# Kernel tuning notes

Measured on AMD Instinct MI355X. Metric: run time of the kernel, lower is better.

Reference implementation:

```python
import jax, jax.numpy as jnp
import numpy as np

B, D, O = 512, 256, 256
H = [512, 1024, 1024]

def _linear_params(key, fan_in, fan_out):
    kw, kb = jax.random.split(key)
    bound = 1.0 / np.sqrt(fan_in)
    W = jax.random.uniform(kw, (fan_out, fan_in), jnp.float32, -bound, bound)
    b = jax.random.uniform(kb, (fan_out,), jnp.float32, -bound, bound)
    return W, b

def setup_inputs() -> dict:
    key = jax.random.key(0)
    ks = jax.random.split(key, 7)
    input_values = jax.random.normal(ks[0], (B, D), jnp.float32)
    nan_flag = jax.random.uniform(ks[1], (B, D), jnp.float32)
    W_in, b_in = _linear_params(ks[2], D, H[0])          # input_layer: nan_flag_dim -> H[0]
    W_h1, b_h1 = _linear_params(ks[3], H[0], H[1])        # hidden layer 1
    W_h2, b_h2 = _linear_params(ks[4], H[1], H[2])        # hidden layer 2
    W_d, b_d = _linear_params(ks[5], H[2], D * O)         # output_branch_dense
    W_b, b_b = _linear_params(ks[6], H[2], O)             # output_branch_bias
    return {"input_values": input_values, "nan_flag": nan_flag, "training": False,
            "W_in": W_in, "b_in": b_in, "W_h1": W_h1, "b_h1": b_h1,
            "W_h2": W_h2, "b_h2": b_h2, "W_d": W_d, "b_d": b_d,
            "W_b": W_b, "b_b": b_b}

def reference(input_values, nan_flag, training, W_in, b_in, W_h1, b_h1, W_h2, b_h2, W_d, b_d, W_b, b_b):
    # training=False: dropout is identity, sample_missing branch skipped (default False)
    x = jax.nn.relu(nan_flag @ W_in.T + b_in)
    x = jax.nn.relu(x @ W_h1.T + b_h1)
    x = jax.nn.relu(x @ W_h2.T + b_h2)
    # per-sample compensation weights [B, D, O] and bias [B, O]
    comp_w = (x @ W_d.T + b_d).reshape(B, D, O)
    comp_b = x @ W_b.T + b_b
    # baddbmm: [B,1,D] @ [B,D,O] + [B,1,O] -> squeeze -> [B,O]
    out = comp_b + jnp.einsum('bd,bdo->bo', input_values, comp_w)
    return out
```

## Files before the change

### kernel.cpp

```cpp
#include <hip/hip_runtime.h>
#include <hip/hip_bf16.h>

#define B_  512
#define D_  256
#define O_  256
#define H2_ 1024

typedef __attribute__((ext_vector_type(4))) float  f32x4;
typedef __attribute__((ext_vector_type(8))) short  short8;
typedef __attribute__((ext_vector_type(4))) short  short4v;

union S8u { short4v v; unsigned u[2]; };

__device__ __forceinline__ unsigned f32_bf16(float x) {
  unsigned u = __builtin_bit_cast(unsigned, x);
  return (u + 0x7fffu + ((u >> 16) & 1u)) >> 16;
}
__device__ __forceinline__ unsigned cvt_pk_bf16(float a, float b) {
  return f32_bf16(a) | (f32_bf16(b) << 16);
}

template <int RELU>
__global__ __launch_bounds__(256)
void gemm_bt64(const float* __restrict__ A, const float* __restrict__ Bm,
               const float* __restrict__ bias, float* __restrict__ C,
               int M, int N, int K) {
  __shared__ __align__(16) short As[64][72];
  __shared__ __align__(16) short Bs[64][72];
  const int t    = threadIdx.x;
  const int m0   = blockIdx.y * 64;
  const int n0   = blockIdx.x * 64;
  const int f4c  = t & 15;
  const int rg   = t >> 4;
  const int lane = t & 63;
  const int w    = t >> 6;
  const int wm   = (w & 1) * 32;
  const int wn   = (w >> 1) * 32;
  const int lr   = lane & 15;
  const int lq   = lane >> 4;

  f32x4 acc[2][2];
  #pragma unroll
  for (int i = 0; i < 2; ++i)
    #pragma unroll
    for (int j = 0; j < 2; ++j) acc[i][j] = f32x4{0.f, 0.f, 0.f, 0.f};

  for (int k0 = 0; k0 < K; k0 += 64) {
    #pragma unroll
    for (int j = 0; j < 4; ++j) {
      int r = rg + 16 * j;
      f32x4 av = *(const f32x4*)(A  + (size_t)(m0 + r) * K + k0 + f4c * 4);
      f32x4 bv = *(const f32x4*)(Bm + (size_t)(n0 + r) * K + k0 + f4c * 4);
      S8u sa; sa.u[0] = cvt_pk_bf16(av.x, av.y); sa.u[1] = cvt_pk_bf16(av.z, av.w);
      S8u sb; sb.u[0] = cvt_pk_bf16(bv.x, bv.y); sb.u[1] = cvt_pk_bf16(bv.z, bv.w);
      *(short4v*)&As[r][f4c * 4] = sa.v;
      *(short4v*)&Bs[r][f4c * 4] = sb.v;
    }
    __syncthreads();
    #pragma unroll
    for (int ks = 0; ks < 2; ++ks) {
      short8 a0 = *(const short8*)&As[wm + lr     ][ks * 32 + lq * 8];
      short8 a1 = *(const short8*)&As[wm + 16 + lr][ks * 32 + lq * 8];
      short8 b0 = *(const short8*)&Bs[wn + lr     ][ks * 32 + lq * 8];
      short8 b1 = *(const short8*)&Bs[wn + 16 + lr][ks * 32 + lq * 8];
      acc[0][0] = __builtin_amdgcn_mfma_f32_16x16x32_bf16(a0, b0, acc[0][0], 0, 0, 0);
      acc[0][1] = __builtin_amdgcn_mfma_f32_16x16x32_bf16(a0, b1, acc[0][1], 0, 0, 0);
      acc[1][0] = __builtin_amdgcn_mfma_f32_16x16x32_bf16(a1, b0, acc[1][0], 0, 0, 0);
      acc[1][1] = __builtin_amdgcn_mfma_f32_16x16x32_bf16(a1, b1, acc[1][1], 0, 0, 0);
    }
    __syncthreads();
  }
  #pragma unroll
  for (int mi = 0; mi < 2; ++mi)
    #pragma unroll
    for (int ni = 0; ni < 2; ++ni)
      #pragma unroll
      for (int r = 0; r < 4; ++r) {
        int row = m0 + wm + mi * 16 + lq * 4 + r;
        int col = n0 + wn + ni * 16 + lr;
        float v = acc[mi][ni][r] + bias[col];
        if (RELU) v = fmaxf(v, 0.f);
        C[(size_t)row * N + col] = v;
      }
}

__global__ __launch_bounds__(256)
void bias_d_kernel(const float* __restrict__ inp, const float* __restrict__ b_d,
                   float* __restrict__ out) {
  const int b = blockIdx.x;
  const int o = threadIdx.x;
  const float* ir = inp + (size_t)b * D_;
  float s = 0.f;
  for (int d = 0; d < D_; ++d)
    s += ir[d] * b_d[(size_t)d * O_ + o];
  out[(size_t)b * O_ + o] += s;
}

__global__ __launch_bounds__(256, 2)
void stage_b(const float* __restrict__ x2, const float* __restrict__ inp,
             const float* __restrict__ Wd, float* __restrict__ out) {
  __shared__ __align__(16) short As[128][72];
  __shared__ __align__(16) short Bs[128][72];
  const int t    = threadIdx.x;
  const int mt   = blockIdx.x >> 1;
  const int nt   = blockIdx.x & 1;
  const int d0   = blockIdx.y * 4;
  const int bm   = mt * 128;
  const int bn   = nt * 128;
  const int f4c  = t & 15;
  const int rg   = t >> 4;
  const int lane = t & 63;
  const int w    = t >> 6;
  const int wm   = (w & 1) * 64;
  const int wn   = (w >> 1) * 64;
  const int lr   = lane & 15;
  const int lq   = lane >> 4;

  f32x4 acc[4][4];
  #pragma unroll
  for (int mi = 0; mi < 4; ++mi)
    #pragma unroll
    for (int ni = 0; ni < 4; ++ni) acc[mi][ni] = f32x4{0.f, 0.f, 0.f, 0.f};

  for (int dl = 0; dl < 4; ++dl) {
    const int d = d0 + dl;
    float insc[8];
    #pragma unroll
    for (int j = 0; j < 8; ++j)
      insc[j] = inp[(size_t)(bm + rg + 16 * j) * D_ + d];
    const float* wbase = Wd + ((size_t)d * O_ + bn) * H2_;

    for (int h0 = 0; h0 < H2_; h0 += 64) {
      #pragma unroll
      for (int j = 0; j < 8; ++j) {
        int r = rg + 16 * j;
        f32x4 xv = *(const f32x4*)(x2 + (size_t)(bm + r) * H2_ + h0 + f4c * 4);
        float s = insc[j];
        S8u sa;
        sa.u[0] = cvt_pk_bf16(xv.x * s, xv.y * s);
        sa.u[1] = cvt_pk_bf16(xv.z * s, xv.w * s);
        *(short4v*)&As[r][f4c * 4] = sa.v;
        f32x4 wv = *(const f32x4*)(wbase + (size_t)r * H2_ + h0 + f4c * 4);
        S8u sb; sb.u[0] = cvt_pk_bf16(wv.x, wv.y); sb.u[1] = cvt_pk_bf16(wv.z, wv.w);
        *(short4v*)&Bs[r][f4c * 4] = sb.v;
      }
      __syncthreads();
      #pragma unroll
      for (int ks = 0; ks < 2; ++ks) {
        short8 af[4], bfr[4];
        #pragma unroll
        for (int mi = 0; mi < 4; ++mi)
          af[mi] = *(const short8*)&As[wm + mi * 16 + lr][ks * 32 + lq * 8];
        #pragma unroll
        for (int ni = 0; ni < 4; ++ni)
          bfr[ni] = *(const short8*)&Bs[wn + ni * 16 + lr][ks * 32 + lq * 8];
        #pragma unroll
        for (int mi = 0; mi < 4; ++mi)
          #pragma unroll
          for (int ni = 0; ni < 4; ++ni)
            acc[mi][ni] = __builtin_amdgcn_mfma_f32_16x16x32_bf16(af[mi], bfr[ni],
                                                                  acc[mi][ni], 0, 0, 0);
      }
      __syncthreads();
    }
  }

  #pragma unroll
  for (int mi = 0; mi < 4; ++mi)
    #pragma unroll
    for (int ni = 0; ni < 4; ++ni)
      #pragma unroll
      for (int r = 0; r < 4; ++r) {
        int row = bm + wm + mi * 16 + lq * 4 + r;
        int col = bn + wn + ni * 16 + lr;
        atomicAdd(out + (size_t)row * O_ + col, acc[mi][ni][r]);
      }
}

extern "C" void kernel_launch(void* const* d_in, const int* in_sizes, int n_in,
                              void* d_out, int out_size, void* d_ws, size_t ws_size,
                              hipStream_t stream) {
  const float* input = (const float*)d_in[0];
  const float* nanf  = (const float*)d_in[1];
  const float* W_in  = (const float*)d_in[3];
  const float* b_in  = (const float*)d_in[4];
  const float* W_h1  = (const float*)d_in[5];
  const float* b_h1  = (const float*)d_in[6];
  const float* W_h2  = (const float*)d_in[7];
  const float* b_h2  = (const float*)d_in[8];
  const float* W_d   = (const float*)d_in[9];
  const float* b_d   = (const float*)d_in[10];
  const float* W_b   = (const float*)d_in[11];
  const float* b_b   = (const float*)d_in[12];
  float* out = (float*)d_out;

  float* x0 = (float*)d_ws;
  float* x1 = x0 + 512 * 512;
  float* x2 = x1 + 512 * 1024;

  gemm_bt64<1><<<dim3(512 / 64, 512 / 64), 256, 0, stream>>>(nanf, W_in, b_in, x0, 512, 512, 256);
  gemm_bt64<1><<<dim3(1024 / 64, 512 / 64), 256, 0, stream>>>(x0, W_h1, b_h1, x1, 512, 1024, 512);
  gemm_bt64<1><<<dim3(1024 / 64, 512 / 64), 256, 0, stream>>>(x1, W_h2, b_h2, x2, 512, 1024, 1024);
  gemm_bt64<0><<<dim3(256 / 64, 512 / 64), 256, 0, stream>>>(x2, W_b, b_b, out, 512, 256, 1024);
  bias_d_kernel<<<512, 256, 0, stream>>>(input, b_d, out);
  stage_b<<<dim3(8, 64), 256, 0, stream>>>(x2, input, W_d, out);
}
```

Baseline: 630.3 us.

## Pre-convert W_d and x2 to bf16 and stream via global_load_lds in stage_b

Adds a conversion kernel that turns W_d (256 MB fp32) and x2 into bf16 copies in the workspace each call. The main stage then loads tiles directly into LDS with global_load_lds instead of converting fp32 in registers. The input scaling moves from the A operand to a per-d epilogue that accumulates scaled partial results. The conversion pass reads all of W_d and writes a 128 MB copy, which adds traffic unless it is cheaper than the fp32 reads it replaces. The fast path only runs if the workspace is large enough, otherwise the old kernel is used.

After: 647.9 us. +2.8%, slower.

```diff
diff --git a/kernel.cpp b/kernel.cpp
--- a/kernel.cpp
+++ b/kernel.cpp
@@ -1,5 +1,4 @@
 #include <hip/hip_runtime.h>
-#include <hip/hip_bf16.h>
 
 #define B_  512
 #define D_  256
@@ -9,8 +8,10 @@
 typedef __attribute__((ext_vector_type(4))) float  f32x4;
 typedef __attribute__((ext_vector_type(8))) short  short8;
 typedef __attribute__((ext_vector_type(4))) short  short4v;
-
-union S8u { short4v v; unsigned u[2]; };
+typedef unsigned short ushort_t;
+
+union S8u  { short4v v; unsigned u[2]; };
+union S16u { short8  v; unsigned u[4]; };
 
 __device__ __forceinline__ unsigned f32_bf16(float x) {
   unsigned u = __builtin_bit_cast(unsigned, x);
@@ -18,6 +19,12 @@
 }
 __device__ __forceinline__ unsigned cvt_pk_bf16(float a, float b) {
   return f32_bf16(a) | (f32_bf16(b) << 16);
+}
+
+__device__ __forceinline__ void gload_lds16(const void* g, void* l) {
+  __builtin_amdgcn_global_load_lds(
+      (const __attribute__((address_space(1))) unsigned*)g,
+      (__attribute__((address_space(3))) unsigned*)l, 16, 0, 0);
 }
 
 template <int RELU>
@@ -96,9 +103,116 @@
   out[(size_t)b * O_ + o] += s;
 }
 
+__global__ __launch_bounds__(256)
+void cvt_f32_bf16(const float* __restrict__ in, ushort_t* __restrict__ out, int n8) {
+  for (size_t i = (size_t)blockIdx.x * 256 + threadIdx.x; i < (size_t)n8;
+       i += (size_t)gridDim.x * 256) {
+    const float* p = in + i * 8;
+    f32x4 v0 = *(const f32x4*)p;
+    f32x4 v1 = *(const f32x4*)(p + 4);
+    S16u s;
+    s.u[0] = cvt_pk_bf16(v0.x, v0.y);
+    s.u[1] = cvt_pk_bf16(v0.z, v0.w);
+    s.u[2] = cvt_pk_bf16(v1.x, v1.y);
+    s.u[3] = cvt_pk_bf16(v1.z, v1.w);
+    *(short8*)(out + i * 8) = s.v;
+  }
+}
+
 __global__ __launch_bounds__(256, 2)
-void stage_b(const float* __restrict__ x2, const float* __restrict__ inp,
-             const float* __restrict__ Wd, float* __restrict__ out) {
+void stage_b2(const ushort_t* __restrict__ x2b, const float* __restrict__ inp,
+              const ushort_t* __restrict__ Wdb, float* __restrict__ out) {
+  __shared__ __align__(16) ushort_t As[128 * 64];
+  __shared__ __align__(16) ushort_t Bs[128 * 64];
+  const int t    = threadIdx.x;
+  const int lin  = blockIdx.x + 8 * blockIdx.y;
+  const int mt   = lin >> 7;
+  const int g    = lin & 127;
+  const int nt   = g & 1;
+  const int y    = g >> 1;
+  const int bm   = mt * 128;
+  const int bn   = nt * 128;
+  const int d0   = y * 4;
+  const int lane = t & 63;
+  const int w    = t >> 6;
+  const int wm   = (w & 1) * 64;
+  const int wn   = (w >> 1) * 64;
+  const int lr   = lane & 15;
+  const int lq   = lane >> 4;
+  const int srow = w * 32 + (lane >> 3);
+  const int scol = (lane & 7) * 8;
+
+  f32x4 run[4][4];
+  #pragma unroll
+  for (int mi = 0; mi < 4; ++mi)
+    #pragma unroll
+    for (int ni = 0; ni < 4; ++ni) run[mi][ni] = f32x4{0.f, 0.f, 0.f, 0.f};
+
+  for (int dl = 0; dl < 4; ++dl) {
+    const int d = d0 + dl;
+    const ushort_t* wrow = Wdb + (size_t)(d * O_ + bn) * H2_;
+
+    f32x4 acc[4][4];
+    #pragma unroll
+    for (int mi = 0; mi < 4; ++mi)
+      #pragma unroll
+      for (int ni = 0; ni < 4; ++ni) acc[mi][ni] = f32x4{0.f, 0.f, 0.f, 0.f};
+
+    for (int h0 = 0; h0 < H2_; h0 += 64) {
+      #pragma unroll
+      for (int c = 0; c < 4; ++c) {
+        const int r = srow + c * 8;
+        gload_lds16(x2b  + (size_t)(bm + r) * H2_ + h0 + scol,
+                    &As[(w * 32 + c * 8) * 64]);
+        gload_lds16(wrow + (size_t)r * H2_ + h0 + scol,
+                    &Bs[(w * 32 + c * 8) * 64]);
+      }
+      __syncthreads();
+      #pragma unroll
+      for (int ks = 0; ks < 2; ++ks) {
+        short8 af[4], bfr[4];
+        #pragma unroll
+        for (int mi = 0; mi < 4; ++mi)
+          af[mi] = *(const short8*)&As[(wm + mi * 16 + lr) * 64 + ks * 32 + lq * 8];
+        #pragma unroll
+        for (int ni = 0; ni < 4; ++ni)
+          bfr[ni] = *(const short8*)&Bs[(wn + ni * 16 + lr) * 64 + ks * 32 + lq * 8];
+        #pragma unroll
+        for (int mi = 0; mi < 4; ++mi)
+          #pragma unroll
+          for (int ni = 0; ni < 4; ++ni)
+            acc[mi][ni] = __builtin_amdgcn_mfma_f32_16x16x32_bf16(af[mi], bfr[ni],
+                                                                  acc[mi][ni], 0, 0, 0);
+      }
+      __syncthreads();
+    }
+
+    #pragma unroll
+    for (int mi = 0; mi < 4; ++mi)
+      #pragma unroll
+      for (int r = 0; r < 4; ++r) {
+        const float sc = inp[(size_t)(bm + wm + mi * 16 + lq * 4 + r) * D_ + d];
+        #pragma unroll
+        for (int ni = 0; ni < 4; ++ni)
+          run[mi][ni][r] += sc * acc[mi][ni][r];
+      }
+  }
+
+  #pragma unroll
+  for (int mi = 0; mi < 4; ++mi)
+    #pragma unroll
+    for (int ni = 0; ni < 4; ++ni)
+      #pragma unroll
+      for (int r = 0; r < 4; ++r) {
+        int row = bm + wm + mi * 16 + lq * 4 + r;
+        int col = bn + wn + ni * 16 + lr;
+        atomicAdd(out + (size_t)row * O_ + col, run[mi][ni][r]);
+      }
+}
+
+__global__ __launch_bounds__(256, 2)
+void stage_b_old(const float* __restrict__ x2, const float* __restrict__ inp,
+                 const float* __restrict__ Wd, float* __restrict__ out) {
   __shared__ __align__(16) short As[128][72];
   __shared__ __align__(16) short Bs[128][72];
   const int t    = threadIdx.x;
@@ -197,11 +311,23 @@
   float* x0 = (float*)d_ws;
   float* x1 = x0 + 512 * 512;
   float* x2 = x1 + 512 * 1024;
+  ushort_t* x2b = (ushort_t*)(x2 + 512 * 1024);
+  ushort_t* Wdb = (ushort_t*)((char*)d_ws + 6ull * 1024 * 1024);
+  const size_t need = 6ull * 1024 * 1024 + 134217728ull;
+  const bool fast = ws_size >= need;
+
+  if (fast)
+    cvt_f32_bf16<<<2048, 256, 0, stream>>>(W_d, Wdb, 65536 * 1024 / 8);
 
   gemm_bt64<1><<<dim3(512 / 64, 512 / 64), 256, 0, stream>>>(nanf, W_in, b_in, x0, 512, 512, 256);
   gemm_bt64<1><<<dim3(1024 / 64, 512 / 64), 256, 0, stream>>>(x0, W_h1, b_h1, x1, 512, 1024, 512);
   gemm_bt64<1><<<dim3(1024 / 64, 512 / 64), 256, 0, stream>>>(x1, W_h2, b_h2, x2, 512, 1024, 1024);
+  if (fast)
+    cvt_f32_bf16<<<256, 256, 0, stream>>>(x2, x2b, 512 * 1024 / 8);
   gemm_bt64<0><<<dim3(256 / 64, 512 / 64), 256, 0, stream>>>(x2, W_b, b_b, out, 512, 256, 1024);
   bias_d_kernel<<<512, 256, 0, stream>>>(input, b_d, out);
-  stage_b<<<dim3(8, 64), 256, 0, stream>>>(x2, input, W_d, out);
-}
+  if (fast)
+    stage_b2<<<dim3(8, 64), 256, 0, stream>>>(x2b, input, Wdb, out);
+  else
+    stage_b_old<<<dim3(8, 64), 256, 0, stream>>>(x2, input, W_d, out);
+}
```

## Restructure dense-branch GEMM: defer input scaling to epilogue, bf16 x2, double-buffered LDS

Applied to the files above, without the earlier changes.

The stage-B kernel no longer multiplies x2 by each input value before every GEMM. It computes the unscaled x2·W_d products for 16 d-values and 16 outputs per tile, then applies the input_values weighting in the epilogue. x2 is converted to bf16 once in a separate kernel and streamed into double-buffered, swizzled LDS via global_load_lds, while W_d is prefetched two steps ahead in registers. Each output element now takes one atomic add per block instead of one per MFMA output, and the repeated x2 reloads and conversions are removed. The cost is more accumulator registers (512-thread blocks, 4x8 MFMA tiles) and hand-placed waitcnt/barrier scheduling that must stay correct.

New measurement: 603.2 us. -4.3%, faster.

```diff
diff --git a/kernel.cpp b/kernel.cpp
--- a/kernel.cpp
+++ b/kernel.cpp
@@ -1,5 +1,4 @@
 #include <hip/hip_runtime.h>
-#include <hip/hip_bf16.h>
 
 #define B_  512
 #define D_  256
@@ -9,8 +8,10 @@
 typedef __attribute__((ext_vector_type(4))) float  f32x4;
 typedef __attribute__((ext_vector_type(8))) short  short8;
 typedef __attribute__((ext_vector_type(4))) short  short4v;
-
-union S8u { short4v v; unsigned u[2]; };
+typedef unsigned short ushort_t;
+
+union S8u  { short4v v; unsigned u[2]; };
+union S16u { short8  v; unsigned u[4]; };
 
 __device__ __forceinline__ unsigned f32_bf16(float x) {
   unsigned u = __builtin_bit_cast(unsigned, x);
@@ -18,6 +19,12 @@
 }
 __device__ __forceinline__ unsigned cvt_pk_bf16(float a, float b) {
   return f32_bf16(a) | (f32_bf16(b) << 16);
+}
+
+__device__ __forceinline__ void gload_lds16(const void* g, void* l) {
+  __builtin_amdgcn_global_load_lds(
+      (const __attribute__((address_space(1))) unsigned*)g,
+      (__attribute__((address_space(3))) unsigned*)l, 16, 0, 0);
 }
 
 template <int RELU>
@@ -96,85 +103,154 @@
   out[(size_t)b * O_ + o] += s;
 }
 
-__global__ __launch_bounds__(256, 2)
-void stage_b(const float* __restrict__ x2, const float* __restrict__ inp,
-             const float* __restrict__ Wd, float* __restrict__ out) {
-  __shared__ __align__(16) short As[128][72];
-  __shared__ __align__(16) short Bs[128][72];
+__global__ __launch_bounds__(256)
+void cvt_f32_bf16(const float* __restrict__ in, ushort_t* __restrict__ out, int n8) {
+  for (size_t i = (size_t)blockIdx.x * 256 + threadIdx.x; i < (size_t)n8;
+       i += (size_t)gridDim.x * 256) {
+    const float* p = in + i * 8;
+    f32x4 v0 = *(const f32x4*)p;
+    f32x4 v1 = *(const f32x4*)(p + 4);
+    S16u s;
+    s.u[0] = cvt_pk_bf16(v0.x, v0.y);
+    s.u[1] = cvt_pk_bf16(v0.z, v0.w);
+    s.u[2] = cvt_pk_bf16(v1.x, v1.y);
+    s.u[3] = cvt_pk_bf16(v1.z, v1.w);
+    *(short8*)(out + i * 8) = s.v;
+  }
+}
+
+__global__ __launch_bounds__(512, 2)
+void stage_b4(const ushort_t* __restrict__ x2b, const float* __restrict__ inp,
+              const float* __restrict__ Wd, float* __restrict__ out) {
+  __shared__ __align__(16) ushort_t As[2][256 * 32];
+  __shared__ __align__(16) ushort_t Bs[2][256 * 32];
   const int t    = threadIdx.x;
-  const int mt   = blockIdx.x >> 1;
-  const int nt   = blockIdx.x & 1;
-  const int d0   = blockIdx.y * 4;
-  const int bm   = mt * 128;
-  const int bn   = nt * 128;
-  const int f4c  = t & 15;
-  const int rg   = t >> 4;
+  const int lin  = blockIdx.x + 8 * blockIdx.y;
+  const int mt   = lin >> 8;
+  const int nb   = lin & 255;
+  const int d0   = (nb >> 4) * 16;
+  const int og   = (nb & 15) * 16;
+  const int bm   = mt * 256;
   const int lane = t & 63;
   const int w    = t >> 6;
-  const int wm   = (w & 1) * 64;
-  const int wn   = (w >> 1) * 64;
+  const int wm   = (w >> 1) * 64;
+  const int wn   = (w & 1) * 128;
   const int lr   = lane & 15;
   const int lq   = lane >> 4;
 
-  f32x4 acc[4][4];
+  const int arow = lane >> 2;
+  const int aswz = (lane & 3) ^ ((lane >> 3) & 3);
+  const ushort_t* a_src0 = x2b + (size_t)(bm + (w & 3) * 0) * 0;
+  const ushort_t* aptr[2];
+  #pragma unroll
+  for (int c = 0; c < 2; ++c)
+    aptr[c] = x2b + (size_t)(bm + w * 32 + c * 16 + arow) * H2_ + aswz * 8;
+
+  const int rr = t >> 1;
+  const int hh = t & 1;
+  const int wr = (d0 + (rr >> 4)) * 256 + og + (rr & 15);
+  const float* bptr = Wd + (size_t)wr * H2_ + hh * 16;
+  const int bsw = (rr >> 1) & 3;
+
+  const int sl = (lq ^ ((lr >> 1) & 3)) * 8;
+
+  f32x4 acc[4][8];
   #pragma unroll
   for (int mi = 0; mi < 4; ++mi)
     #pragma unroll
-    for (int ni = 0; ni < 4; ++ni) acc[mi][ni] = f32x4{0.f, 0.f, 0.f, 0.f};
-
-  for (int dl = 0; dl < 4; ++dl) {
-    const int d = d0 + dl;
-    float insc[8];
-    #pragma unroll
-    for (int j = 0; j < 8; ++j)
-      insc[j] = inp[(size_t)(bm + rg + 16 * j) * D_ + d];
-    const float* wbase = Wd + ((size_t)d * O_ + bn) * H2_;
-
-    for (int h0 = 0; h0 < H2_; h0 += 64) {
+    for (int nj = 0; nj < 8; ++nj) acc[mi][nj] = f32x4{0.f, 0.f, 0.f, 0.f};
+
+  f32x4 breg[4];
+
+  auto stageA = [&](int k, int bf) {
+    #pragma unroll
+    for (int c = 0; c < 2; ++c)
+      gload_lds16(aptr[c] + k * 32, &As[bf][(w * 32 + c * 16) * 32]);
+  };
+  auto loadB = [&](int k) {
+    const float* p = bptr + k * 32;
+    breg[0] = *(const f32x4*)p;
+    breg[1] = *(const f32x4*)(p + 4);
+    breg[2] = *(const f32x4*)(p + 8);
+    breg[3] = *(const f32x4*)(p + 12);
+  };
+  auto writeB = [&](int bf) {
+    S16u s0, s1;
+    s0.u[0] = cvt_pk_bf16(breg[0].x, breg[0].y);
+    s0.u[1] = cvt_pk_bf16(breg[0].z, breg[0].w);
+    s0.u[2] = cvt_pk_bf16(breg[1].x, breg[1].y);
+    s0.u[3] = cvt_pk_bf16(breg[1].z, breg[1].w);
+    s1.u[0] = cvt_pk_bf16(breg[2].x, breg[2].y);
+    s1.u[1] = cvt_pk_bf16(breg[2].z, breg[2].w);
+    s1.u[2] = cvt_pk_bf16(breg[3].x, breg[3].y);
+    s1.u[3] = cvt_pk_bf16(breg[3].z, breg[3].w);
+    const int lcg0 = hh * 2;
+    *(short8*)&Bs[bf][rr * 32 + (lcg0 ^ bsw) * 8]       = s0.v;
+    *(short8*)&Bs[bf][rr * 32 + ((lcg0 + 1) ^ bsw) * 8] = s1.v;
+  };
+
+  stageA(0, 0);
+  __builtin_amdgcn_sched_barrier(0);
+  loadB(0);
+  __builtin_amdgcn_sched_barrier(0);
+  asm volatile("s_waitcnt vmcnt(0)" ::: "memory");
+  writeB(0);
+  loadB(1);
+  __builtin_amdgcn_sched_barrier(0);
+  asm volatile("s_waitcnt lgkmcnt(0)" ::: "memory");
+  __builtin_amdgcn_s_barrier();
+
+  int buf = 0;
+  for (int k = 0; k < 32; ++k) {
+    if (k < 31) {
+      stageA(k + 1, buf ^ 1);
+      __builtin_amdgcn_sched_barrier(0);
+      asm volatile("s_waitcnt vmcnt(2)" ::: "memory");
+      writeB(buf ^ 1);
+    }
+    if (k < 30) {
+      loadB(k + 2);
+      __builtin_amdgcn_sched_barrier(0);
+    }
+
+    short8 af[4], bf[8];
+    #pragma unroll
+    for (int mi = 0; mi < 4; ++mi)
+      af[mi] = *(const short8*)&As[buf][(wm + mi * 16 + lr) * 32 + sl];
+    #pragma unroll
+    for (int nj = 0; nj < 8; ++nj)
+      bf[nj] = *(const short8*)&Bs[buf][(wn + nj * 16 + lr) * 32 + sl];
+    #pragma unroll
+    for (int mi = 0; mi < 4; ++mi)
       #pragma unroll
-      for (int j = 0; j < 8; ++j) {
-        int r = rg + 16 * j;
-        f32x4 xv = *(const f32x4*)(x2 + (size_t)(bm + r) * H2_ + h0 + f4c * 4);
-        float s = insc[j];
-        S8u sa;
-        sa.u[0] = cvt_pk_bf16(xv.x * s, xv.y * s);
-        sa.u[1] = cvt_pk_bf16(xv.z * s, xv.w * s);
-        *(short4v*)&As[r][f4c * 4] = sa.v;
-        f32x4 wv = *(const f32x4*)(wbase + (size_t)r * H2_ + h0 + f4c * 4);
-        S8u sb; sb.u[0] = cvt_pk_bf16(wv.x, wv.y); sb.u[1] = cvt_pk_bf16(wv.z, wv.w);
-        *(short4v*)&Bs[r][f4c * 4] = sb.v;
-      }
-      __syncthreads();
-      #pragma unroll
-      for (int ks = 0; ks < 2; ++ks) {
-        short8 af[4], bfr[4];
-        #pragma unroll
-        for (int mi = 0; mi < 4; ++mi)
-          af[mi] = *(const short8*)&As[wm + mi * 16 + lr][ks * 32 + lq * 8];
-        #pragma unroll
-        for (int ni = 0; ni < 4; ++ni)
-          bfr[ni] = *(const short8*)&Bs[wn + ni * 16 + lr][ks * 32 + lq * 8];
-        #pragma unroll
-        for (int mi = 0; mi < 4; ++mi)
-          #pragma unroll
-          for (int ni = 0; ni < 4; ++ni)
-            acc[mi][ni] = __builtin_amdgcn_mfma_f32_16x16x32_bf16(af[mi], bfr[ni],
-                                                                  acc[mi][ni], 0, 0, 0);
-      }
-      __syncthreads();
+      for (int nj = 0; nj < 8; ++nj)
+        acc[mi][nj] = __builtin_amdgcn_mfma_f32_16x16x32_bf16(af[mi], bf[nj],
+                                                              acc[mi][nj], 0, 0, 0);
+
+    if (k < 31) {
+      if (k < 30) { asm volatile("s_waitcnt vmcnt(4)" ::: "memory"); }
+      else        { asm volatile("s_waitcnt vmcnt(0)" ::: "memory"); }
+      asm volatile("s_waitcnt lgkmcnt(0)" ::: "memory");
+      __builtin_amdgcn_s_barrier();
+      buf ^= 1;
     }
   }
 
+  const int dbase = d0 + (w & 1) * 8;
+  const int o     = og + lr;
   #pragma unroll
   for (int mi = 0; mi < 4; ++mi)
     #pragma unroll
-    for (int ni = 0; ni < 4; ++ni)
-      #pragma unroll
-      for (int r = 0; r < 4; ++r) {
-        int row = bm + wm + mi * 16 + lq * 4 + r;
-        int col = bn + wn + ni * 16 + lr;
-        atomicAdd(out + (size_t)row * O_ + col, acc[mi][ni][r]);
-      }
+    for (int r = 0; r < 4; ++r) {
+      const int row = bm + wm + mi * 16 + lq * 4 + r;
+      f32x4 s0 = *(const f32x4*)(inp + (size_t)row * D_ + dbase);
+      f32x4 s1 = *(const f32x4*)(inp + (size_t)row * D_ + dbase + 4);
+      float v = s0.x * acc[mi][0][r] + s0.y * acc[mi][1][r] +
+                s0.z * acc[mi][2][r] + s0.w * acc[mi][3][r] +
+                s1.x * acc[mi][4][r] + s1.y * acc[mi][5][r] +
+                s1.z * acc[mi][6][r] + s1.w * acc[mi][7][r];
+      atomicAdd(out + (size_t)row * O_ + o, v);
+    }
 }
 
 extern "C" void kernel_launch(void* const* d_in, const int* in_sizes, int n_in,
@@ -197,11 +273,13 @@
   float* x0 = (float*)d_ws;
   float* x1 = x0 + 512 * 512;
   float* x2 = x1 + 512 * 1024;
+  ushort_t* x2b = (ushort_t*)(x2 + 512 * 1024);
 
   gemm_bt64<1><<<dim3(512 / 64, 512 / 64), 256, 0, stream>>>(nanf, W_in, b_in, x0, 512, 512, 256);
   gemm_bt64<1><<<dim3(1024 / 64, 512 / 64), 256, 0, stream>>>(x0, W_h1, b_h1, x1, 512, 1024, 512);
   gemm_bt64<1><<<dim3(1024 / 64, 512 / 64), 256, 0, stream>>>(x1, W_h2, b_h2, x2, 512, 1024, 1024);
+  cvt_f32_bf16<<<256, 256, 0, stream>>>(x2, x2b, 512 * 1024 / 8);
   gemm_bt64<0><<<dim3(256 / 64, 512 / 64), 256, 0, stream>>>(x2, W_b, b_b, out, 512, 256, 1024);
   bias_d_kernel<<<512, 256, 0, stream>>>(input, b_d, out);
-  stage_b<<<dim3(8, 64), 256, 0, stream>>>(x2, input, W_d, out);
-}
+  stage_b4<<<dim3(8, 64), 512, 0, stream>>>(x2b, input, W_d, out);
+}
```
